# Kernel tuning notes

Hardware: AMD Instinct MI355X
Metric: run time of the kernel (lower is better)

Reference implementation:

```python
import jax, jax.numpy as jnp
import numpy as np

B, T, D = 8, 2048, 1024
GAMMA = 0.96875


def setup_inputs() -> dict:
    key = jax.random.key(0)
    ks = jax.random.split(key, 7)
    sD = 1.0 / np.sqrt(D)
    sT = 1.0 / np.sqrt(T)
    return {
        "x": jax.random.normal(ks[0], (B, T, D), dtype=jnp.float32),
        "Wq": jax.random.normal(ks[1], (D, D), dtype=jnp.float32) * sD,
        "Wk": jax.random.normal(ks[2], (D, D), dtype=jnp.float32) * sD,
        "Wv": jax.random.normal(ks[3], (D, D), dtype=jnp.float32) * sD,
        "W_ih": jax.random.normal(ks[4], (T, T), dtype=jnp.float32) * sT,
        "W_hh": jax.random.normal(ks[5], (T, T), dtype=jnp.float32) * sT,
        "b_ih": jax.random.normal(ks[6], (T,), dtype=jnp.float32) * sT,
    }


def reference(x, Wq, Wk, Wv, W_ih, W_hh, b_ih):
    # x: [B, T, D]; QKV projections (Linear with no bias: x @ W^T)
    Q = jnp.einsum("btd,ed->bte", x, Wq)
    K = jnp.einsum("btd,ed->bte", x, Wk)
    V = jnp.einsum("btd,ed->bte", x, Wv)

    # retention state injected as hidden bias of the tanh-RNN: [B, T]
    bias = jnp.sum(K * V, axis=-1)

    gamma = jnp.full((T,), GAMMA, dtype=x.dtype)
    u = gamma @ W_ih.T + b_ih  # input contribution, identical every step: [T]

    def step(h, b_t):
        h_new = jnp.tanh(u + h @ W_hh.T + b_t)
        return h_new, h_new

    h0 = jnp.zeros((T,), dtype=x.dtype)
    _, S = jax.lax.scan(step, h0, bias)  # scan over the B rows -> S: [B, T]

    # vmap(mul)(S, Q^T)^T  ==  out[b,t,d] = S[b,t] * Q[b,t,d]
    return S[:, :, None] * Q
```

## Files before the change

kernel.cpp:

```cpp
#include <hip/hip_runtime.h>
#include <stdint.h>

#define T_DIM 2048
#define D_DIM 1024
#define B_DIM 8
#define M_TOK (B_DIM * T_DIM)
#define GAMMA_C 0.96875f

typedef float f32x4 __attribute__((ext_vector_type(4)));
typedef float f32x16 __attribute__((ext_vector_type(16)));
typedef float fl4 __attribute__((ext_vector_type(4)));
typedef __bf16 bf16x8 __attribute__((ext_vector_type(8)));
typedef unsigned short us8 __attribute__((ext_vector_type(8)));
typedef unsigned short us4 __attribute__((ext_vector_type(4)));

__device__ __forceinline__ unsigned short f32_bf16_rne(float f) {
  uint32_t u = __builtin_bit_cast(uint32_t, f);
  return (unsigned short)((u + 0x7FFFu + ((u >> 16) & 1u)) >> 16);
}
__device__ __forceinline__ float bf16_f32(unsigned short h) {
  uint32_t u = ((uint32_t)h) << 16;
  return __builtin_bit_cast(float, u);
}

__device__ __forceinline__ int swz_row(int r) {
  return ((r >> 1) & 3) ^ ((r >> 3) & 3);
}

__device__ __forceinline__ void gload16(const void* g, void* l) {
  __builtin_amdgcn_global_load_lds(
      reinterpret_cast<const __attribute__((address_space(1))) uint32_t*>(
          reinterpret_cast<uintptr_t>(g)),
      reinterpret_cast<__attribute__((address_space(3))) uint32_t*>(
          reinterpret_cast<uintptr_t>(l)),
      16, 0, 0);
}

__device__ __forceinline__ bf16x8 ldfrag(const unsigned short* p) {
  us8 u = *reinterpret_cast<const us8*>(p);
  return __builtin_bit_cast(bf16x8, u);
}

__global__ __launch_bounds__(256) void k_split(const float* __restrict__ in, int n4,
                                               unsigned short* __restrict__ hi,
                                               unsigned short* __restrict__ lo) {
  int stride = gridDim.x * blockDim.x;
  for (int i = blockIdx.x * blockDim.x + threadIdx.x; i < n4; i += stride) {
    fl4 v = ((const fl4*)in)[i];
    us4 h, l;
#pragma unroll
    for (int j = 0; j < 4; ++j) {
      unsigned short hb = f32_bf16_rne(v[j]);
      float rem = v[j] - bf16_f32(hb);
      h[j] = hb;
      l[j] = f32_bf16_rne(rem);
    }
    ((us4*)hi)[i] = h;
    ((us4*)lo)[i] = l;
  }
}

__global__ __launch_bounds__(256) void k_split_hi(const float* __restrict__ in, int n4,
                                                  unsigned short* __restrict__ hi) {
  int stride = gridDim.x * blockDim.x;
  for (int i = blockIdx.x * blockDim.x + threadIdx.x; i < n4; i += stride) {
    fl4 v = ((const fl4*)in)[i];
    us4 h;
#pragma unroll
    for (int j = 0; j < 4; ++j) h[j] = f32_bf16_rne(v[j]);
    ((us4*)hi)[i] = h;
  }
}

__global__ __launch_bounds__(256) void k_split_T(const float* __restrict__ in,
                                                 unsigned short* __restrict__ th,
                                                 unsigned short* __restrict__ tl) {
  __shared__ float tile[64][69];
  int be = blockIdx.x >> 4, bd = blockIdx.x & 15;
  int e0 = be * 64, d0 = bd * 64;
  int r = threadIdx.x >> 4;
  int c = (threadIdx.x & 15) * 4;
#pragma unroll
  for (int it = 0; it < 4; ++it) {
    int rr = r + it * 16;
    fl4 v = *(const fl4*)(in + (size_t)(e0 + rr) * D_DIM + d0 + c);
#pragma unroll
    for (int j = 0; j < 4; ++j) tile[rr][c + j] = v[j];
  }
  __syncthreads();
#pragma unroll
  for (int it = 0; it < 4; ++it) {
    int dr = r + it * 16;
    us4 h, l;
#pragma unroll
    for (int j = 0; j < 4; ++j) {
      float f = tile[c + j][dr];
      h[j] = f32_bf16_rne(f);
      l[j] = f32_bf16_rne(f - bf16_f32(h[j]));
    }
    *(us4*)(th + (size_t)(d0 + dr) * D_DIM + e0 + c) = h;
    *(us4*)(tl + (size_t)(d0 + dr) * D_DIM + e0 + c) = l;
  }
}

__global__ __launch_bounds__(256) void k_u(const float* __restrict__ Wih,
                                           const float* __restrict__ bih,
                                           float* __restrict__ u) {
  int wave = threadIdx.x >> 6, lane = threadIdx.x & 63;
  int t = blockIdx.x * 4 + wave;
  const fl4* row = (const fl4*)(Wih + (size_t)t * T_DIM);
  float s = 0.f;
#pragma unroll
  for (int i = 0; i < 8; ++i) {
    fl4 v = row[lane + i * 64];
    s += v[0] + v[1] + v[2] + v[3];
  }
#pragma unroll
  for (int m = 32; m >= 1; m >>= 1) s += __shfl_xor(s, m, 64);
  if (lane == 0) u[t] = GAMMA_C * s + bih[t];
}

__global__ __launch_bounds__(256) void k_step_bf(const unsigned short* __restrict__ Whh_b,
                                                 const float* __restrict__ hprev,
                                                 const float* __restrict__ u,
                                                 const float* __restrict__ biasrow,
                                                 float* __restrict__ hout) {
  int wave = threadIdx.x >> 6, lane = threadIdx.x & 63;
  int t = blockIdx.x * 4 + wave;
  const unsigned short* row = Whh_b + (size_t)t * T_DIM;
  float s = 0.f;
#pragma unroll
  for (int i = 0; i < 4; ++i) {
    us8 w = *(const us8*)(row + i * 512 + lane * 8);
    fl4 h0 = *(const fl4*)(hprev + i * 512 + lane * 8);
    fl4 h1 = *(const fl4*)(hprev + i * 512 + lane * 8 + 4);
    s += bf16_f32(w[0]) * h0[0] + bf16_f32(w[1]) * h0[1] +
         bf16_f32(w[2]) * h0[2] + bf16_f32(w[3]) * h0[3] +
         bf16_f32(w[4]) * h1[0] + bf16_f32(w[5]) * h1[1] +
         bf16_f32(w[6]) * h1[2] + bf16_f32(w[7]) * h1[3];
  }
#pragma unroll
  for (int m = 32; m >= 1; m >>= 1) s += __shfl_xor(s, m, 64);
  if (lane == 0) hout[t] = tanhf(u[t] + s + biasrow[t]);
}

__device__ __forceinline__ void map_blk(int bid, int& mb, int& nb) {
  int sw = (bid & 7) * 128 + (bid >> 3);
  mb = sw >> 3;
  nb = sw & 7;
}

__global__ __launch_bounds__(256) void k_ht(
    const unsigned short* __restrict__ ah, const unsigned short* __restrict__ al,
    const unsigned short* __restrict__ bh, const unsigned short* __restrict__ bl,
    unsigned short* __restrict__ outh, unsigned short* __restrict__ outl) {
  __shared__ unsigned short sAh[2][64 * 32], sAl[2][64 * 32];
  __shared__ unsigned short sBh[2][64 * 32], sBl[2][64 * 32];
  const int tid = threadIdx.x;
  const int wave = tid >> 6, lane = tid & 63;
  const int wm = wave >> 1, wn = wave & 1;
  const int m0 = (blockIdx.x >> 4) * 64, n0 = (blockIdx.x & 15) * 64;
  const int hi32 = lane >> 5;

  const int srow = tid >> 2;
  const int csrc = (tid & 3) ^ swz_row(srow);
  const size_t ga = (size_t)(m0 + srow) * D_DIM + csrc * 8;
  const size_t gb = (size_t)(n0 + srow) * D_DIM + csrc * 8;
  const int ldst = tid * 8;

  f32x16 acc = {};
  const int l31 = lane & 31;
  const int sw = swz_row(l31);
  const int ar = wm * 32 + l31;
  const int br = wn * 32 + l31;
  int aoff[2], boff[2];
#pragma unroll
  for (int kh = 0; kh < 2; ++kh) {
    aoff[kh] = ar * 32 + (((kh * 2 + hi32) ^ sw) * 8);
    boff[kh] = br * 32 + (((kh * 2 + hi32) ^ sw) * 8);
  }

#define HT_STAGE(t, buf)                         \
  do {                                           \
    const size_t ko = (size_t)(t) * 32;          \
    gload16(ah + ga + ko, &sAh[buf][ldst]);      \
    gload16(al + ga + ko, &sAl[buf][ldst]);      \
    gload16(bh + gb + ko, &sBh[buf][ldst]);      \
    gload16(bl + gb + ko, &sBl[buf][ldst]);      \
  } while (0)

  HT_STAGE(0, 0);
  __syncthreads();
  for (int kt = 0; kt < 32; ++kt) {
    const int cur = kt & 1;
    if (kt < 31) HT_STAGE(kt + 1, cur ^ 1);
#pragma unroll
    for (int kh = 0; kh < 2; ++kh) {
      bf16x8 fah = ldfrag(&sAh[cur][aoff[kh]]);
      bf16x8 fal = ldfrag(&sAl[cur][aoff[kh]]);
      bf16x8 fbh = ldfrag(&sBh[cur][boff[kh]]);
      bf16x8 fbl = ldfrag(&sBl[cur][boff[kh]]);
      acc = __builtin_amdgcn_mfma_f32_32x32x16_bf16(fah, fbh, acc, 0, 0, 0);
      acc = __builtin_amdgcn_mfma_f32_32x32x16_bf16(fah, fbl, acc, 0, 0, 0);
      acc = __builtin_amdgcn_mfma_f32_32x32x16_bf16(fal, fbh, acc, 0, 0, 0);
    }
    __syncthreads();
  }
#pragma unroll
  for (int r = 0; r < 16; ++r) {
    int row = m0 + wm * 32 + (r & 3) + 8 * (r >> 2) + 4 * hi32;
    int col = n0 + wn * 32 + l31;
    float f = acc[r];
    unsigned short hb = f32_bf16_rne(f);
    unsigned short lb = f32_bf16_rne(f - bf16_f32(hb));
    size_t ad = (size_t)row * D_DIM + col;
    outh[ad] = hb;
    outl[ad] = lb;
  }
#undef HT_STAGE
}

__global__ __launch_bounds__(256, 2) void k_y_bias(
    const unsigned short* __restrict__ xh, const unsigned short* __restrict__ xl,
    const unsigned short* __restrict__ bh, const unsigned short* __restrict__ bl,
    const float* __restrict__ xf, float* __restrict__ bias) {
  __shared__ unsigned short sAh[2][128 * 32], sAl[2][128 * 32];
  __shared__ unsigned short sBh[2][128 * 32], sBl[2][128 * 32];
  const int tid = threadIdx.x;
  const int wave = tid >> 6, lane = tid & 63;
  const int wm = wave >> 1, wn = wave & 1;
  int mb, nb;
  map_blk(blockIdx.x, mb, nb);
  const int m0 = mb * 128, n0 = nb * 128;
  const int hi32 = lane >> 5;

  const int srow0 = tid >> 2, srow1 = srow0 + 64;
  const int csrc0 = (tid & 3) ^ swz_row(srow0);
  const int csrc1 = (tid & 3) ^ swz_row(srow1);
  const size_t gaA0 = (size_t)(m0 + srow0) * D_DIM + csrc0 * 8;
  const size_t gaA1 = (size_t)(m0 + srow1) * D_DIM + csrc1 * 8;
  const size_t gaB0 = (size_t)(n0 + srow0) * D_DIM + csrc0 * 8;
  const size_t gaB1 = (size_t)(n0 + srow1) * D_DIM + csrc1 * 8;
  const int ldst0 = tid * 8, ldst1 = (tid + 256) * 8;

  f32x16 acc[2][2] = {};
  const int l31 = lane & 31;
  const int sw = swz_row(l31);
  int aoff[2][2], boff[2][2];
#pragma unroll
  for (int mi = 0; mi < 2; ++mi) {
    int r = wm * 64 + mi * 32 + l31;
#pragma unroll
    for (int kh = 0; kh < 2; ++kh)
      aoff[mi][kh] = r * 32 + (((kh * 2 + hi32) ^ sw) * 8);
  }
#pragma unroll
  for (int ni = 0; ni < 2; ++ni) {
    int r = wn * 64 + ni * 32 + l31;
#pragma unroll
    for (int kh = 0; kh < 2; ++kh)
      boff[ni][kh] = r * 32 + (((kh * 2 + hi32) ^ sw) * 8);
  }

#define Y_STAGE(t, buf)                           \
  do {                                            \
    const size_t ko = (size_t)(t) * 32;           \
    gload16(xh + gaA0 + ko, &sAh[buf][ldst0]);    \
    gload16(xh + gaA1 + ko, &sAh[buf][ldst1]);    \
    gload16(xl + gaA0 + ko, &sAl[buf][ldst0]);    \
    gload16(xl + gaA1 + ko, &sAl[buf][ldst1]);    \
    gload16(bh + gaB0 + ko, &sBh[buf][ldst0]);    \
    gload16(bh + gaB1 + ko, &sBh[buf][ldst1]);    \
    gload16(bl + gaB0 + ko, &sBl[buf][ldst0]);    \
    gload16(bl + gaB1 + ko, &sBl[buf][ldst1]);    \
  } while (0)

  Y_STAGE(0, 0);
  __syncthreads();
  for (int kt = 0; kt < 32; ++kt) {
    const int cur = kt & 1;
    if (kt < 31) Y_STAGE(kt + 1, cur ^ 1);
#pragma unroll
    for (int kh = 0; kh < 2; ++kh) {
      bf16x8 fah[2], fal[2], fbh_[2], fbl_[2];
#pragma unroll
      for (int mi = 0; mi < 2; ++mi) {
        fah[mi] = ldfrag(&sAh[cur][aoff[mi][kh]]);
        fal[mi] = ldfrag(&sAl[cur][aoff[mi][kh]]);
      }
#pragma unroll
      for (int ni = 0; ni < 2; ++ni) {
        fbh_[ni] = ldfrag(&sBh[cur][boff[ni][kh]]);
        fbl_[ni] = ldfrag(&sBl[cur][boff[ni][kh]]);
      }
      __builtin_amdgcn_s_setprio(1);
#pragma unroll
      for (int mi = 0; mi < 2; ++mi)
#pragma unroll
        for (int ni = 0; ni < 2; ++ni) {
          acc[mi][ni] = __builtin_amdgcn_mfma_f32_32x32x16_bf16(fah[mi], fbh_[ni], acc[mi][ni], 0, 0, 0);
          acc[mi][ni] = __builtin_amdgcn_mfma_f32_32x32x16_bf16(fah[mi], fbl_[ni], acc[mi][ni], 0, 0, 0);
          acc[mi][ni] = __builtin_amdgcn_mfma_f32_32x32x16_bf16(fal[mi], fbh_[ni], acc[mi][ni], 0, 0, 0);
        }
      __builtin_amdgcn_s_setprio(0);
    }
    __syncthreads();
  }

#pragma unroll
  for (int mi = 0; mi < 2; ++mi)
#pragma unroll
    for (int r = 0; r < 16; ++r) {
      int row = m0 + wm * 64 + mi * 32 + (r & 3) + 8 * (r >> 2) + 4 * hi32;
      const float* xr = xf + (size_t)row * D_DIM + n0 + wn * 64 + l31;
      float p = xr[0] * acc[mi][0][r] + xr[32] * acc[mi][1][r];
      p += __shfl_xor(p, 1, 64);
      p += __shfl_xor(p, 2, 64);
      p += __shfl_xor(p, 4, 64);
      p += __shfl_xor(p, 8, 64);
      p += __shfl_xor(p, 16, 64);
      if (l31 == 0) atomicAdd(&bias[row], p);
    }
#undef Y_STAGE
}

__global__ __launch_bounds__(256, 4) void k_q_out(
    const unsigned short* __restrict__ xh,
    const unsigned short* __restrict__ qh_,
    const float* __restrict__ S, float* __restrict__ out) {
  __shared__ unsigned short sA[2][128 * 32];
  __shared__ unsigned short sB[2][128 * 32];
  const int tid = threadIdx.x;
  const int wave = tid >> 6, lane = tid & 63;
  const int wm = wave >> 1, wn = wave & 1;
  int mb, nb;
  map_blk(blockIdx.x, mb, nb);
  const int m0 = mb * 128, n0 = nb * 128;
  const int hi32 = lane >> 5;

  const int srow0 = tid >> 2, srow1 = srow0 + 64;
  const int csrc0 = (tid & 3) ^ swz_row(srow0);
  const int csrc1 = (tid & 3) ^ swz_row(srow1);
  const size_t gaA0 = (size_t)(m0 + srow0) * D_DIM + csrc0 * 8;
  const size_t gaA1 = (size_t)(m0 + srow1) * D_DIM + csrc1 * 8;
  const size_t gaB0 = (size_t)(n0 + srow0) * D_DIM + csrc0 * 8;
  const size_t gaB1 = (size_t)(n0 + srow1) * D_DIM + csrc1 * 8;
  const int ldst0 = tid * 8, ldst1 = (tid + 256) * 8;

  f32x16 acc[2][2] = {};
  const int l31 = lane & 31;
  const int sw = swz_row(l31);
  int aoff[2][2], boff[2][2];
#pragma unroll
  for (int mi = 0; mi < 2; ++mi) {
    int r = wm * 64 + mi * 32 + l31;
#pragma unroll
    for (int kh = 0; kh < 2; ++kh)
      aoff[mi][kh] = r * 32 + (((kh * 2 + hi32) ^ sw) * 8);
  }
#pragma unroll
  for (int ni = 0; ni < 2; ++ni) {
    int r = wn * 64 + ni * 32 + l31;
#pragma unroll
    for (int kh = 0; kh < 2; ++kh)
      boff[ni][kh] = r * 32 + (((kh * 2 + hi32) ^ sw) * 8);
  }

#define Q_STAGE(t, buf)                           \
  do {                                            \
    const size_t ko = (size_t)(t) * 32;           \
    gload16(xh + gaA0 + ko, &sA[buf][ldst0]);     \
    gload16(xh + gaA1 + ko, &sA[buf][ldst1]);     \
    gload16(qh_ + gaB0 + ko, &sB[buf][ldst0]);    \
    gload16(qh_ + gaB1 + ko, &sB[buf][ldst1]);    \
  } while (0)

  Q_STAGE(0, 0);
  __syncthreads();
  for (int kt = 0; kt < 32; ++kt) {
    const int cur = kt & 1;
    if (kt < 31) Q_STAGE(kt + 1, cur ^ 1);
#pragma unroll
    for (int kh = 0; kh < 2; ++kh) {
      bf16x8 fa[2], fb[2];
#pragma unroll
      for (int mi = 0; mi < 2; ++mi) fa[mi] = ldfrag(&sA[cur][aoff[mi][kh]]);
#pragma unroll
      for (int ni = 0; ni < 2; ++ni) fb[ni] = ldfrag(&sB[cur][boff[ni][kh]]);
      __builtin_amdgcn_s_setprio(1);
#pragma unroll
      for (int mi = 0; mi < 2; ++mi)
#pragma unroll
        for (int ni = 0; ni < 2; ++ni)
          acc[mi][ni] = __builtin_amdgcn_mfma_f32_32x32x16_bf16(fa[mi], fb[ni], acc[mi][ni], 0, 0, 0);
      __builtin_amdgcn_s_setprio(0);
    }
    __syncthreads();
  }

#pragma unroll
  for (int mi = 0; mi < 2; ++mi)
#pragma unroll
    for (int r = 0; r < 16; ++r) {
      int row = m0 + wm * 64 + mi * 32 + (r & 3) + 8 * (r >> 2) + 4 * hi32;
      float sc = S[row];
      float* orow = out + (size_t)row * D_DIM + n0 + wn * 64 + l31;
      orow[0] = sc * acc[mi][0][r];
      orow[32] = sc * acc[mi][1][r];
    }
#undef Q_STAGE
}

extern "C" void kernel_launch(void* const* d_in, const int* in_sizes, int n_in,
                              void* d_out, int out_size, void* d_ws, size_t ws_size,
                              hipStream_t stream) {
  const float* x   = (const float*)d_in[0];
  const float* Wq  = (const float*)d_in[1];
  const float* Wk  = (const float*)d_in[2];
  const float* Wv  = (const float*)d_in[3];
  const float* Wih = (const float*)d_in[4];
  const float* Whh = (const float*)d_in[5];
  const float* bih = (const float*)d_in[6];
  float* out = (float*)d_out;

  char* ws = (char*)d_ws;
  size_t off = 0;
  auto alloc = [&](size_t bytes) -> char* {
    char* p = ws + off;
    off += (bytes + 255) & ~(size_t)255;
    return p;
  };
  unsigned short* xh   = (unsigned short*)alloc((size_t)M_TOK * D_DIM * 2);
  unsigned short* xl   = (unsigned short*)alloc((size_t)M_TOK * D_DIM * 2);
  unsigned short* wqh  = (unsigned short*)alloc((size_t)D_DIM * D_DIM * 2);
  unsigned short* wkth = (unsigned short*)alloc((size_t)D_DIM * D_DIM * 2);
  unsigned short* wktl = (unsigned short*)alloc((size_t)D_DIM * D_DIM * 2);
  unsigned short* wvth = (unsigned short*)alloc((size_t)D_DIM * D_DIM * 2);
  unsigned short* wvtl = (unsigned short*)alloc((size_t)D_DIM * D_DIM * 2);
  unsigned short* hth  = (unsigned short*)alloc((size_t)D_DIM * D_DIM * 2);
  unsigned short* htl  = (unsigned short*)alloc((size_t)D_DIM * D_DIM * 2);
  float* bias = (float*)alloc((size_t)M_TOK * 4);
  float* Sbuf = (float*)alloc((size_t)M_TOK * 4);
  float* ubuf = (float*)alloc((size_t)T_DIM * 4);
  float* zbuf = (float*)alloc((size_t)T_DIM * 4);
  unsigned short* whhb = wkth;
  (void)ws_size; (void)in_sizes; (void)n_in; (void)out_size;

  k_split<<<2048, 256, 0, stream>>>(x, M_TOK * D_DIM / 4, xh, xl);
  k_split_hi<<<512, 256, 0, stream>>>(Wq, D_DIM * D_DIM / 4, wqh);
  k_split_T<<<256, 256, 0, stream>>>(Wk, wkth, wktl);
  k_split_T<<<256, 256, 0, stream>>>(Wv, wvth, wvtl);

  hipMemsetAsync(bias, 0, (size_t)M_TOK * 4, stream);
  hipMemsetAsync(zbuf, 0, (size_t)T_DIM * 4, stream);

  k_u<<<T_DIM / 4, 256, 0, stream>>>(Wih, bih, ubuf);

  k_ht<<<256, 256, 0, stream>>>(wvth, wvtl, wkth, wktl, hth, htl);

  k_split_hi<<<1024, 256, 0, stream>>>(Whh, T_DIM * T_DIM / 4, whhb);

  k_y_bias<<<1024, 256, 0, stream>>>(xh, xl, hth, htl, x, bias);

  for (int b = 0; b < B_DIM; ++b) {
    const float* hp = (b == 0) ? zbuf : (Sbuf + (size_t)(b - 1) * T_DIM);
    k_step_bf<<<T_DIM / 4, 256, 0, stream>>>(whhb, hp, ubuf, bias + (size_t)b * T_DIM,
                                             Sbuf + (size_t)b * T_DIM);
  }

  k_q_out<<<1024, 256, 0, stream>>>(xh, wqh, Sbuf, out);
}
```

Baseline: 267.2 us.

## Exploit symmetry of bilinear bias form with upper-triangular matrix to skip K-tiles

The bias x·(Wk^T Wv)·x is a quadratic form, so the bias GEMM now uses a symmetrized upper-triangular matrix M' = triu(H + H^T) built by a new k_nprime kernel, and each output block starts its K loop at its column block index. This skips the lower-triangular K-tiles, roughly halving the bias GEMM's MFMA work. It adds one fp32 intermediate buffer and an extra transpose kernel, and gives uneven work across blocks. The split kernels also process eight elements per thread with wider stores.

```diff
diff --git a/kernel.cpp b/kernel.cpp
--- a/kernel.cpp
+++ b/kernel.cpp
@@ -41,34 +41,41 @@
   return __builtin_bit_cast(bf16x8, u);
 }
 
-__global__ __launch_bounds__(256) void k_split(const float* __restrict__ in, int n4,
+__global__ __launch_bounds__(256) void k_split(const float* __restrict__ in, int n8,
                                                unsigned short* __restrict__ hi,
                                                unsigned short* __restrict__ lo) {
   int stride = gridDim.x * blockDim.x;
-  for (int i = blockIdx.x * blockDim.x + threadIdx.x; i < n4; i += stride) {
-    fl4 v = ((const fl4*)in)[i];
-    us4 h, l;
+  for (int i = blockIdx.x * blockDim.x + threadIdx.x; i < n8; i += stride) {
+    fl4 v0 = ((const fl4*)in)[i * 2];
+    fl4 v1 = ((const fl4*)in)[i * 2 + 1];
+    us8 h, l;
 #pragma unroll
     for (int j = 0; j < 4; ++j) {
-      unsigned short hb = f32_bf16_rne(v[j]);
-      float rem = v[j] - bf16_f32(hb);
+      unsigned short hb = f32_bf16_rne(v0[j]);
       h[j] = hb;
-      l[j] = f32_bf16_rne(rem);
-    }
-    ((us4*)hi)[i] = h;
-    ((us4*)lo)[i] = l;
-  }
-}
-
-__global__ __launch_bounds__(256) void k_split_hi(const float* __restrict__ in, int n4,
+      l[j] = f32_bf16_rne(v0[j] - bf16_f32(hb));
+      unsigned short hb1 = f32_bf16_rne(v1[j]);
+      h[j + 4] = hb1;
+      l[j + 4] = f32_bf16_rne(v1[j] - bf16_f32(hb1));
+    }
+    ((us8*)hi)[i] = h;
+    ((us8*)lo)[i] = l;
+  }
+}
+
+__global__ __launch_bounds__(256) void k_split_hi(const float* __restrict__ in, int n8,
                                                   unsigned short* __restrict__ hi) {
   int stride = gridDim.x * blockDim.x;
-  for (int i = blockIdx.x * blockDim.x + threadIdx.x; i < n4; i += stride) {
-    fl4 v = ((const fl4*)in)[i];
-    us4 h;
-#pragma unroll
-    for (int j = 0; j < 4; ++j) h[j] = f32_bf16_rne(v[j]);
-    ((us4*)hi)[i] = h;
+  for (int i = blockIdx.x * blockDim.x + threadIdx.x; i < n8; i += stride) {
+    fl4 v0 = ((const fl4*)in)[i * 2];
+    fl4 v1 = ((const fl4*)in)[i * 2 + 1];
+    us8 h;
+#pragma unroll
+    for (int j = 0; j < 4; ++j) {
+      h[j] = f32_bf16_rne(v0[j]);
+      h[j + 4] = f32_bf16_rne(v1[j]);
+    }
+    ((us8*)hi)[i] = h;
   }
 }
 
@@ -153,7 +160,7 @@
 __global__ __launch_bounds__(256) void k_ht(
     const unsigned short* __restrict__ ah, const unsigned short* __restrict__ al,
     const unsigned short* __restrict__ bh, const unsigned short* __restrict__ bl,
-    unsigned short* __restrict__ outh, unsigned short* __restrict__ outl) {
+    float* __restrict__ Hf) {
   __shared__ unsigned short sAh[2][64 * 32], sAl[2][64 * 32];
   __shared__ unsigned short sBh[2][64 * 32], sBl[2][64 * 32];
   const int tid = threadIdx.x;
@@ -210,14 +217,49 @@
   for (int r = 0; r < 16; ++r) {
     int row = m0 + wm * 32 + (r & 3) + 8 * (r >> 2) + 4 * hi32;
     int col = n0 + wn * 32 + l31;
-    float f = acc[r];
-    unsigned short hb = f32_bf16_rne(f);
-    unsigned short lb = f32_bf16_rne(f - bf16_f32(hb));
-    size_t ad = (size_t)row * D_DIM + col;
-    outh[ad] = hb;
-    outl[ad] = lb;
+    Hf[(size_t)row * D_DIM + col] = acc[r];
   }
 #undef HT_STAGE
+}
+
+__global__ __launch_bounds__(256) void k_nprime(const float* __restrict__ Hf,
+                                                unsigned short* __restrict__ mh,
+                                                unsigned short* __restrict__ ml) {
+  __shared__ float t2[64][65];
+  const int ti = blockIdx.x >> 4;
+  const int tj = blockIdx.x & 15;
+  const int r0 = ti * 64, c0 = tj * 64;
+  const int a = threadIdx.x >> 2;
+  const int b4 = (threadIdx.x & 3) * 16;
+  if (tj < ti) {
+#pragma unroll
+    for (int j = 0; j < 16; ++j) {
+      size_t ad = (size_t)(r0 + a) * D_DIM + c0 + b4 + j;
+      mh[ad] = 0;
+      ml[ad] = 0;
+    }
+    return;
+  }
+#pragma unroll
+  for (int j = 0; j < 16; j += 4) {
+    fl4 v = *(const fl4*)(Hf + (size_t)(c0 + a) * D_DIM + r0 + b4 + j);
+#pragma unroll
+    for (int q = 0; q < 4; ++q) t2[a][b4 + j + q] = v[q];
+  }
+  __syncthreads();
+#pragma unroll
+  for (int j = 0; j < 16; ++j) {
+    int dp = r0 + a;
+    int dd = c0 + b4 + j;
+    float v = 0.f;
+    if (dd > dp)       v = Hf[(size_t)dp * D_DIM + dd] + t2[b4 + j][a];
+    else if (dd == dp) v = Hf[(size_t)dp * D_DIM + dd];
+    unsigned short hb = f32_bf16_rne(v);
+    unsigned short lb = f32_bf16_rne(v - bf16_f32(hb));
+    size_t ad = (size_t)dp * D_DIM + dd;
+    mh[ad] = hb;
+    ml[ad] = lb;
+  }
 }
 
 __global__ __launch_bounds__(256, 2) void k_y_bias(
@@ -233,6 +275,7 @@
   map_blk(blockIdx.x, mb, nb);
   const int m0 = mb * 128, n0 = nb * 128;
   const int hi32 = lane >> 5;
+  const int kt0 = nb * 4;
 
   const int srow0 = tid >> 2, srow1 = srow0 + 64;
   const int csrc0 = (tid & 3) ^ swz_row(srow0);
@@ -275,10 +318,10 @@
     gload16(bl + gaB1 + ko, &sBl[buf][ldst1]);    \
   } while (0)
 
-  Y_STAGE(0, 0);
+  Y_STAGE(kt0, 0);
   __syncthreads();
-  for (int kt = 0; kt < 32; ++kt) {
-    const int cur = kt & 1;
+  for (int kt = kt0; kt < 32; ++kt) {
+    const int cur = (kt - kt0) & 1;
     if (kt < 31) Y_STAGE(kt + 1, cur ^ 1);
 #pragma unroll
     for (int kh = 0; kh < 2; ++kh) {
@@ -437,8 +480,9 @@
   unsigned short* wktl = (unsigned short*)alloc((size_t)D_DIM * D_DIM * 2);
   unsigned short* wvth = (unsigned short*)alloc((size_t)D_DIM * D_DIM * 2);
   unsigned short* wvtl = (unsigned short*)alloc((size_t)D_DIM * D_DIM * 2);
-  unsigned short* hth  = (unsigned short*)alloc((size_t)D_DIM * D_DIM * 2);
-  unsigned short* htl  = (unsigned short*)alloc((size_t)D_DIM * D_DIM * 2);
+  unsigned short* mph  = (unsigned short*)alloc((size_t)D_DIM * D_DIM * 2);
+  unsigned short* mpl  = (unsigned short*)alloc((size_t)D_DIM * D_DIM * 2);
+  float* Hf   = (float*)alloc((size_t)D_DIM * D_DIM * 4);
   float* bias = (float*)alloc((size_t)M_TOK * 4);
   float* Sbuf = (float*)alloc((size_t)M_TOK * 4);
   float* ubuf = (float*)alloc((size_t)T_DIM * 4);
@@ -446,8 +490,8 @@
   unsigned short* whhb = wkth;
   (void)ws_size; (void)in_sizes; (void)n_in; (void)out_size;
 
-  k_split<<<2048, 256, 0, stream>>>(x, M_TOK * D_DIM / 4, xh, xl);
-  k_split_hi<<<512, 256, 0, stream>>>(Wq, D_DIM * D_DIM / 4, wqh);
+  k_split<<<2048, 256, 0, stream>>>(x, M_TOK * D_DIM / 8, xh, xl);
+  k_split_hi<<<512, 256, 0, stream>>>(Wq, D_DIM * D_DIM / 8, wqh);
   k_split_T<<<256, 256, 0, stream>>>(Wk, wkth, wktl);
   k_split_T<<<256, 256, 0, stream>>>(Wv, wvth, wvtl);
 
@@ -456,11 +500,13 @@
 
   k_u<<<T_DIM / 4, 256, 0, stream>>>(Wih, bih, ubuf);
 
-  k_ht<<<256, 256, 0, stream>>>(wvth, wvtl, wkth, wktl, hth, htl);
-
-  k_split_hi<<<1024, 256, 0, stream>>>(Whh, T_DIM * T_DIM / 4, whhb);
-
-  k_y_bias<<<1024, 256, 0, stream>>>(xh, xl, hth, htl, x, bias);
+  k_ht<<<256, 256, 0, stream>>>(wvth, wvtl, wkth, wktl, Hf);
+
+  k_nprime<<<256, 256, 0, stream>>>(Hf, mph, mpl);
+
+  k_split_hi<<<1024, 256, 0, stream>>>(Whh, T_DIM * T_DIM / 8, whhb);
+
+  k_y_bias<<<1024, 256, 0, stream>>>(xh, xl, mph, mpl, x, bias);
 
   for (int b = 0; b < B_DIM; ++b) {
     const float* hp = (b == 0) ? zbuf : (Sbuf + (size_t)(b - 1) * T_DIM);
```

Measured after the change: 261.7 us. 1.02x faster.
